# Performance work log

Measured on AMD Instinct MI355X. Metric: run time of the kernel, lower is better.

Reference implementation:

```python
import jax, jax.numpy as jnp
import numpy as np

B, P, L = 32, 256, 32            # samples, max paths/sample, tokens/path
V, DE, DP = 30000, 256, 256      # vocab, node emb dim, path emb dim
NH, DH = 8, 32                   # heads, head dim (NH*DH == DP)
DFF = 1024
NLAYERS = 4
MAXCHILD = 32
NEG = -1e9


def setup_inputs() -> dict:
    key = jax.random.key(0)
    ks = jax.random.split(key, 32)
    s = 0.02
    inp = {}
    inp['tokens'] = jax.random.randint(ks[0], (B, P, L), 0, V, dtype=jnp.int32)
    inp['paths_count'] = jax.random.randint(ks[1], (B,), 2, P + 1, dtype=jnp.int32)
    inp['target_indices'] = jax.random.randint(ks[2], (B,), 0, MAXCHILD, dtype=jnp.int32)
    inp['emb'] = jax.random.normal(ks[3], (V, DE)) * s
    inp['lstm1_k'] = jax.random.normal(ks[4], (DE, 4 * DP)) * s
    inp['lstm1_r'] = jax.random.normal(ks[5], (DP, 4 * DP)) * s
    inp['lstm1_b'] = jnp.zeros((4 * DP,))
    inp['lstm2_k'] = jax.random.normal(ks[6], (DP, 4 * DP)) * s
    inp['lstm2_r'] = jax.random.normal(ks[7], (DP, 4 * DP)) * s
    inp['lstm2_b'] = jnp.zeros((4 * DP,))
    inp['enc_wq'] = jax.random.normal(ks[8], (NLAYERS, DP, DP)) * s
    inp['enc_wk'] = jax.random.normal(ks[9], (NLAYERS, DP, DP)) * s
    inp['enc_wv'] = jax.random.normal(ks[10], (NLAYERS, DP, DP)) * s
    inp['enc_wo'] = jax.random.normal(ks[11], (NLAYERS, DP, DP)) * s
    inp['enc_ln1_g'] = jnp.ones((NLAYERS, DP))
    inp['enc_ln1_b'] = jnp.zeros((NLAYERS, DP))
    inp['enc_w1'] = jax.random.normal(ks[12], (NLAYERS, DP, DFF)) * s
    inp['enc_b1'] = jnp.zeros((NLAYERS, DFF))
    inp['enc_w2'] = jax.random.normal(ks[13], (NLAYERS, DFF, DP)) * s
    inp['enc_b2'] = jnp.zeros((NLAYERS, DP))
    inp['enc_ln2_g'] = jnp.ones((NLAYERS, DP))
    inp['enc_ln2_b'] = jnp.zeros((NLAYERS, DP))
    inp['W_r'] = jax.random.normal(ks[14], (DP, DP)) * s
    inp['W_g'] = jax.random.normal(ks[15], (2 * DP, DE)) * s
    inp['C_i'] = jax.random.normal(ks[16], (MAXCHILD, DP, DP)) * s
    return inp


def _lstm(x, K, R, b, return_seq):
    """Keras-style LSTM (gate order i,f,g,o). x: [N, L, d]."""
    N = x.shape[0]
    u = R.shape[0]
    def step(carry, xt):
        h, c = carry
        z = xt @ K + h @ R + b
        i, f, g, o = jnp.split(z, 4, axis=-1)
        c = jax.nn.sigmoid(f) * c + jax.nn.sigmoid(i) * jnp.tanh(g)
        h = jax.nn.sigmoid(o) * jnp.tanh(c)
        return (h, c), (h if return_seq else 0.0)
    init = (jnp.zeros((N, u), x.dtype), jnp.zeros((N, u), x.dtype))
    (h_last, _), ys = jax.lax.scan(step, init, jnp.swapaxes(x, 0, 1))
    return jnp.swapaxes(ys, 0, 1) if return_seq else h_last


def _layernorm(x, g, b):
    m = jnp.mean(x, axis=-1, keepdims=True)
    v = jnp.mean(jnp.square(x - m), axis=-1, keepdims=True)
    return (x - m) * jax.lax.rsqrt(v + 1e-5) * g + b


def _encoder_layer(x, mask, wq, wk, wv, wo, g1, bb1, w1, b1, w2, b2, g2, bb2):
    Bs, n, d = x.shape
    q = (x @ wq).reshape(Bs, n, NH, DH)
    k = (x @ wk).reshape(Bs, n, NH, DH)
    v = (x @ wv).reshape(Bs, n, NH, DH)
    scores = jnp.einsum('bqhd,bkhd->bhqk', q, k) / np.sqrt(DH).astype(np.float32)
    scores = jnp.where(mask[:, None, :, :], scores, NEG)
    a = jax.nn.softmax(scores, axis=-1)
    o = jnp.einsum('bhqk,bkhd->bqhd', a, v).reshape(Bs, n, d) @ wo
    x = _layernorm(x + o, g1, bb1)
    f = jax.nn.relu(x @ w1 + b1) @ w2 + b2
    return _layernorm(x + f, g2, bb2)


def reference(tokens, paths_count, target_indices, emb,
              lstm1_k, lstm1_r, lstm1_b, lstm2_k, lstm2_r, lstm2_b,
              enc_wq, enc_wk, enc_wv, enc_wo, enc_ln1_g, enc_ln1_b,
              enc_w1, enc_b1, enc_w2, enc_b2, enc_ln2_g, enc_ln2_b,
              W_r, W_g, C_i):
    # embed + ragged->flat paths: [B*P, L, DE]
    e = emb[tokens].reshape(B * P, L, DE)
    h1 = _lstm(e, lstm1_k, lstm1_r, lstm1_b, return_seq=True)      # [B*P, L, DP]
    h2 = _lstm(h1, lstm2_k, lstm2_r, lstm2_b, return_seq=False)    # [B*P, DP]
    Hall = h2.reshape(B, P, DP)

    # last valid path per sample is the root context R
    R = Hall[jnp.arange(B), paths_count - 1]                        # [B, DP]
    n = P - 1
    valid = jnp.arange(n)[None, :] < (paths_count - 1)[:, None]     # [B, n]
    H = jnp.where(valid[:, :, None], Hall[:, :n, :], 0.0)           # padded dense, zeros like to_tensor
    mask = valid[:, :, None] & valid[:, None, :]                    # per-sample block mask

    Z = H
    for l in range(NLAYERS):
        Z = _encoder_layer(Z, mask, enc_wq[l], enc_wk[l], enc_wv[l], enc_wo[l],
                           enc_ln1_g[l], enc_ln1_b[l], enc_w1[l], enc_b1[l],
                           enc_w2[l], enc_b2[l], enc_ln2_g[l], enc_ln2_b[l])

    # per-sample transform matrix gather and attention pooling
    C = C_i[target_indices]                                         # [B, DP, DP]
    R = jnp.einsum('bij,bj->bi', C, R)
    R = jax.nn.relu(R) @ W_r                                        # [B, DP]
    alpha = jax.nn.softmax(jnp.einsum('bnd,bd->bn', Z, R), axis=-1) # note: no pad mask (faithful)
    Zp = jnp.einsum('bn,bnd->bd', alpha, Z)                         # [B, DP]
    h = jax.nn.relu(jnp.concatenate([Zp, R], axis=-1) @ W_g)        # [B, DE]
    return jax.nn.softmax(h @ emb.T, axis=-1)                       # [B, V]
```

## Files before the change

kernel.cpp:

```cpp
#include <hip/hip_runtime.h>
#include <cstdint>
#include <cstddef>

typedef unsigned short u16;
typedef unsigned int   u32;
typedef float f32x4 __attribute__((ext_vector_type(4)));
typedef short s16x8 __attribute__((ext_vector_type(8)));
typedef u32   u32x4 __attribute__((ext_vector_type(4)));

#define DEV static __device__ __forceinline__
#define WAIT0SB() do{ asm volatile("s_waitcnt vmcnt(0)" ::: "memory"); __builtin_amdgcn_sched_barrier(0); }while(0)


static constexpr size_t OFF_EMBB = 0;
static constexpr size_t OFF_WP1  = 15360000;
static constexpr size_t OFF_WP2  = 16408576;
static constexpr size_t OFF_BQKV = 17457152;
static constexpr size_t OFF_WOT  = 19030016;
static constexpr size_t OFF_W1ET = 19554304;
static constexpr size_t OFF_W2ET = 21651456;
static constexpr size_t OFF_CIT  = 23748608;
static constexpr size_t OFF_HALL = 32137216;
static constexpr size_t OFF_X    = 40525824;
static constexpr size_t OFF_XB   = 48914432;
static constexpr size_t OFF_Y    = 53108736;
static constexpr size_t OFF_QKV  = 61497344;
static constexpr size_t OFF_AO   = 74080256;
static constexpr size_t OFF_F    = 78274560;
static constexpr size_t OFF_RV   = 95051776;
static constexpr size_t OFF_HB   = 95084544;
static constexpr size_t OFF_LOG  = 95100928;
static constexpr size_t OFF_H1A  = OFF_X;
static constexpr size_t OFF_H1B  = OFF_X + 4194304;
static constexpr size_t OFF_H2A  = OFF_X + 8388608;
static constexpr size_t OFF_H2B  = OFF_X + 12582912;
static constexpr size_t OFF_BARC = OFF_X + 16777216;

DEV u16 f2bf(float f){ u32 u = __builtin_bit_cast(u32, f); u += 0x7fffu + ((u>>16)&1u); return (u16)(u>>16); }
DEV float bf2f(u16 v){ return __builtin_bit_cast(float, (u32)v<<16); }
DEV float sigm(float x){ return 1.f/(1.f+__expf(-x)); }
DEV float tanh_f(float x){ float e=__expf(-2.f*fabsf(x)); float t=(1.f-e)/(1.f+e); return x<0.f? -t:t; }
DEV f32x4 splat4(float x){ f32x4 v={x,x,x,x}; return v; }
DEV f32x4 mfma16(s16x8 a, s16x8 b, f32x4 c){ return __builtin_amdgcn_mfma_f32_16x16x32_bf16(a,b,c,0,0,0); }

DEV int swz256(int row, int col){ int ch=col>>3; return row*256 + (((ch ^ (row&7))&31)<<3) + (col&7); }
DEV int swz128(int row, int col){ int ch=col>>3; return row*128 + (((ch ^ (row&7))&15)<<3) + (col&7); }
DEV int swz32 (int row, int col){ int ch=col>>3; return row*32  + (((ch ^ (row&3))&3)<<3)  + (col&7); }

DEV void st32_s(u32* p, u32 v){
  asm volatile("global_store_dword %0, %1, off sc0 sc1" :: "v"(p), "v"(v) : "memory");
}
DEV u32x4 ld128_s(const u32* p){
  u32x4 r;
  asm volatile("global_load_dwordx4 %0, %1, off sc0 sc1\n\ts_waitcnt vmcnt(0)" : "=v"(r) : "v"(p) : "memory");
  return r;
}
DEV void st128_s(u16* p, s16x8 v){
  asm volatile("global_store_dwordx4 %0, %1, off sc0 sc1" :: "v"(p), "v"(v) : "memory");
}
DEV void ld16_iss(const u16* pa, const u16* pb, s16x8 r[16]){
  asm volatile(
    "global_load_dwordx4 %0, %16, off sc0 sc1\n\t"
    "global_load_dwordx4 %1, %16, off offset:64 sc0 sc1\n\t"
    "global_load_dwordx4 %2, %16, off offset:128 sc0 sc1\n\t"
    "global_load_dwordx4 %3, %16, off offset:192 sc0 sc1\n\t"
    "global_load_dwordx4 %4, %16, off offset:256 sc0 sc1\n\t"
    "global_load_dwordx4 %5, %16, off offset:320 sc0 sc1\n\t"
    "global_load_dwordx4 %6, %16, off offset:384 sc0 sc1\n\t"
    "global_load_dwordx4 %7, %16, off offset:448 sc0 sc1\n\t"
    "global_load_dwordx4 %8, %17, off sc0 sc1\n\t"
    "global_load_dwordx4 %9, %17, off offset:64 sc0 sc1\n\t"
    "global_load_dwordx4 %10, %17, off offset:128 sc0 sc1\n\t"
    "global_load_dwordx4 %11, %17, off offset:192 sc0 sc1\n\t"
    "global_load_dwordx4 %12, %17, off offset:256 sc0 sc1\n\t"
    "global_load_dwordx4 %13, %17, off offset:320 sc0 sc1\n\t"
    "global_load_dwordx4 %14, %17, off offset:384 sc0 sc1\n\t"
    "global_load_dwordx4 %15, %17, off offset:448 sc0 sc1"
    : "=&v"(r[0]),"=&v"(r[1]),"=&v"(r[2]),"=&v"(r[3]),
      "=&v"(r[4]),"=&v"(r[5]),"=&v"(r[6]),"=&v"(r[7]),
      "=&v"(r[8]),"=&v"(r[9]),"=&v"(r[10]),"=&v"(r[11]),
      "=&v"(r[12]),"=&v"(r[13]),"=&v"(r[14]),"=&v"(r[15])
    : "v"(pa), "v"(pb) : "memory");
}

DEV void gbar(u32* arr, u32 gen){
  __syncthreads();
  if (threadIdx.x==0){
    asm volatile("s_waitcnt vmcnt(0)" ::: "memory");
    st32_s(arr + blockIdx.x, gen);
  }
  if (threadIdx.x < 64){
    bool done = false;
    do {
      u32x4 q = ld128_s(arr + threadIdx.x*4);
      done = __all(q.x>=gen && q.y>=gen && q.z>=gen && q.w>=gen);
      if (!done) __builtin_amdgcn_s_sleep(2);
    } while(!done);
  }
  __syncthreads();
}

struct TJob { const float* src; u32 dstOff; int K; int N; int stride; int f32out; };
struct PrepArgs { TJob j[60]; };

__global__ void k_prep(PrepArgs pa, char* __restrict__ ws){
  TJob jb = pa.j[blockIdx.y];
  int tilesK = jb.K >> 5, tilesN = jb.N >> 5;
  int ti = blockIdx.x;
  if (ti >= tilesK*tilesN) return;
  int tk = ti % tilesK, tn = ti / tilesK;
  __shared__ float tile[32][33];
  int r = threadIdx.x >> 5, c = threadIdx.x & 31;
  #pragma unroll
  for (int rr=0; rr<32; rr+=8)
    tile[rr+r][c] = jb.src[(size_t)(tk*32+rr+r)*jb.N + tn*32 + c];
  __syncthreads();
  if (jb.f32out){
    float* dst = (float*)(ws + jb.dstOff);
    #pragma unroll
    for (int rr=0; rr<32; rr+=8)
      dst[(size_t)(tn*32+rr+r)*jb.stride + tk*32 + c] = tile[c][rr+r];
  } else {
    u16* dst = (u16*)(ws + jb.dstOff);
    #pragma unroll
    for (int rr=0; rr<32; rr+=8)
      dst[(size_t)(tn*32+rr+r)*jb.stride + tk*32 + c] = f2bf(tile[c][rr+r]);
  }
}

__global__ void k_embcvt(const float* __restrict__ src, u16* __restrict__ dst, int n4){
  int i = blockIdx.x*blockDim.x + threadIdx.x;
  if (i >= n4) return;
  float4 v = ((const float4*)src)[i];
  uint2 pk;
  pk.x = f2bf(v.x) | ((u32)f2bf(v.y)<<16);
  pk.y = f2bf(v.z) | ((u32)f2bf(v.w)<<16);
  ((uint2*)dst)[i] = pk;
}

__global__ void k_packfrag(const float* __restrict__ srcA, const float* __restrict__ srcB,
                           u16* __restrict__ dst)
{
  int gid = blockIdx.x*256 + threadIdx.x;
  int lane = gid & 63;
  int hs   = (gid>>6) & 15;
  int c    = gid >> 10;
  int kc = c>>2, g = c&3;
  int l4 = lane>>4, l15 = lane&15;
  int col = g*256 + hs*16 + l15;
  int k0  = kc*32 + l4*8;
  u16 out[8];
  #pragma unroll
  for (int j=0;j<8;++j){
    int k = k0 + j;
    float v = (k < 256) ? srcA[(size_t)k*1024 + col] : srcB[(size_t)(k-256)*1024 + col];
    out[j] = f2bf(v);
  }
  *(s16x8*)(dst + (size_t)gid*8) = *(const s16x8*)out;
}

__global__ __launch_bounds__(1024,4) void k_lstm3(
    const int* __restrict__ tokens, const u16* __restrict__ EMBB,
    const u16* __restrict__ WP1, const u16* __restrict__ WP2,
    const float* __restrict__ b1, const float* __restrict__ b2,
    u16* __restrict__ H1A, u16* __restrict__ H1B,
    u16* __restrict__ H2A, u16* __restrict__ H2B,
    u32* __restrict__ bar, float* __restrict__ Hall)
{
  __shared__ u16 W1s[64*512];
  __shared__ u16 W2s[64*512];
  __shared__ u16 Hst[512*16];
  const int tid=threadIdx.x, lane=tid&63, v=tid>>6, l15=lane&15, l4=lane>>4;
  const int bid=blockIdx.x, sg=bid&15, hs=bid>>4;
  const int seq0w = sg*512 + v*32;
  u32* arr = bar;

  #pragma unroll
  for (int i=0;i<4;++i){
    int c = v*4+i;
    const u16* s1 = WP1 + ((size_t)(c*16+hs))*512 + lane*8;
    const u16* s2 = WP2 + ((size_t)(c*16+hs))*512 + lane*8;
    __builtin_amdgcn_global_load_lds((const __attribute__((address_space(1))) void*)s1,
        (__attribute__((address_space(3))) void*)(W1s + c*512), 16, 0, 0);
    __builtin_amdgcn_global_load_lds((const __attribute__((address_space(1))) void*)s2,
        (__attribute__((address_space(3))) void*)(W2s + c*512), 16, 0, 0);
  }
  float bl1[4], bl2[4];
  #pragma unroll
  for (int g=0;g<4;++g){ bl1[g]=b1[g*256 + hs*16 + l15]; bl2[g]=b2[g*256 + hs*16 + l15]; }
  asm volatile("s_waitcnt vmcnt(0)" ::: "memory");
  __syncthreads();

  float c1[8], c2[8];
  #pragma unroll
  for (int i=0;i<8;++i){ c1[i]=0.f; c2[i]=0.f; }
  const int row0 = seq0w + l15, row1 = seq0w + 16 + l15;
  const int cq = tid>>1, chf = tid&1;
  u32 gen = 0;

  #pragma unroll 1
  for (int t=0;t<32;++t){
    const u16* H1r = (t&1)? H1B : H1A;  u16* H1w = (t&1)? H1A : H1B;
    const u16* H2r = (t&1)? H2B : H2A;  u16* H2w = (t&1)? H2A : H2B;
    const int tok0 = tokens[row0*32 + t], tok1 = tokens[row1*32 + t];
    f32x4 acc[2][4];
    s16x8 r[16];
    ld16_iss(H1r + (size_t)row0*256 + l4*8, H1r + (size_t)row1*256 + l4*8, r);
    #pragma unroll
    for (int g=0;g<4;++g){ acc[0][g]=splat4(bl1[g]); acc[1][g]=splat4(bl1[g]); }
    #pragma unroll
    for (int kc=0;kc<8;++kc){
      s16x8 fa0 = *(const s16x8*)(EMBB + (size_t)tok0*256 + kc*32 + l4*8);
      s16x8 fa1 = *(const s16x8*)(EMBB + (size_t)tok1*256 + kc*32 + l4*8);
      #pragma unroll
      for (int g=0;g<4;++g){
        s16x8 wf = *(const s16x8*)&W1s[(kc*4+g)*512 + lane*8];
        acc[0][g]=mfma16(fa0,wf,acc[0][g]);
        acc[1][g]=mfma16(fa1,wf,acc[1][g]);
      }
    }
    WAIT0SB();
    #pragma unroll
    for (int k2=0;k2<8;++k2){
      #pragma unroll
      for (int g=0;g<4;++g){
        s16x8 wf = *(const s16x8*)&W1s[((8+k2)*4+g)*512 + lane*8];
        acc[0][g]=mfma16(r[k2],wf,acc[0][g]);
        acc[1][g]=mfma16(r[8+k2],wf,acc[1][g]);
      }
    }
    #pragma unroll
    for (int m=0;m<2;++m)
      #pragma unroll
      for (int rr=0;rr<4;++rr){
        int idx=m*4+rr;
        float zi=acc[m][0][rr], zf=acc[m][1][rr], zg=acc[m][2][rr], zo=acc[m][3][rr];
        float cc=sigm(zf)*c1[idx]+sigm(zi)*tanh_f(zg);
        c1[idx]=cc;
        Hst[(v*32 + m*16 + l4*4 + rr)*16 + l15] = f2bf(sigm(zo)*tanh_f(cc));
      }
    __syncthreads();
    st128_s(H1w + (size_t)(sg*512 + cq)*256 + hs*16 + chf*8, *(const s16x8*)&Hst[cq*16 + chf*8]);
    ++gen; gbar(arr, gen);
    #pragma unroll
    for (int g=0;g<4;++g){ acc[0][g]=splat4(bl2[g]); acc[1][g]=splat4(bl2[g]); }
    ld16_iss(H1w + (size_t)row0*256 + l4*8, H1w + (size_t)row1*256 + l4*8, r);
    WAIT0SB();
    #pragma unroll
    for (int k2=0;k2<8;++k2){
      #pragma unroll
      for (int g=0;g<4;++g){
        s16x8 wf = *(const s16x8*)&W2s[(k2*4+g)*512 + lane*8];
        acc[0][g]=mfma16(r[k2],wf,acc[0][g]);
        acc[1][g]=mfma16(r[8+k2],wf,acc[1][g]);
      }
    }
    ld16_iss(H2r + (size_t)row0*256 + l4*8, H2r + (size_t)row1*256 + l4*8, r);
    WAIT0SB();
    #pragma unroll
    for (int k2=0;k2<8;++k2){
      #pragma unroll
      for (int g=0;g<4;++g){
        s16x8 wf = *(const s16x8*)&W2s[((8+k2)*4+g)*512 + lane*8];
        acc[0][g]=mfma16(r[k2],wf,acc[0][g]);
        acc[1][g]=mfma16(r[8+k2],wf,acc[1][g]);
      }
    }
    __syncthreads();
    #pragma unroll
    for (int m=0;m<2;++m)
      #pragma unroll
      for (int rr=0;rr<4;++rr){
        int idx=m*4+rr;
        float zi=acc[m][0][rr], zf=acc[m][1][rr], zg=acc[m][2][rr], zo=acc[m][3][rr];
        float cc=sigm(zf)*c2[idx]+sigm(zi)*tanh_f(zg);
        c2[idx]=cc;
        float h=sigm(zo)*tanh_f(cc);
        Hst[(v*32 + m*16 + l4*4 + rr)*16 + l15] = f2bf(h);
        if (t==31) Hall[(size_t)(seq0w + m*16 + l4*4 + rr)*256 + hs*16 + l15] = h;
      }
    __syncthreads();
    st128_s(H2w + (size_t)(sg*512 + cq)*256 + hs*16 + chf*8, *(const s16x8*)&Hst[cq*16 + chf*8]);
  }
}

template<int BM, int EPI>
__global__ __launch_bounds__(512,2) void k_gemm(
    const u16* __restrict__ A, const u16* __restrict__ Bt, void* __restrict__ Cv,
    const float* __restrict__ bias, const float* __restrict__ Res,
    int M, int N, int K, int ldC)
{
  __shared__ u16 Asl[BM*256];
  const int tid=threadIdx.x, lane=tid&63, w=tid>>6, l15=lane&15, l4=lane>>4;
  const int mb=blockIdx.x, nb=blockIdx.y;
  constexpr int MT = BM/16;
  const int col0 = nb*256 + w*32;
  float bz0=0.f, bz1=0.f;
  if (EPI==1 || EPI==3 || EPI==5){ bz0 = bias[col0 + l15]; bz1 = bias[col0 + 16 + l15]; }
  f32x4 acc[MT][2];
  #pragma unroll
  for (int mt=0;mt<MT;++mt){ acc[mt][0]=splat4(bz0); acc[mt][1]=splat4(bz1); }
  for (int kb=0; kb<K; kb+=256){
    __syncthreads();
    if (tid < BM*8){
      int row=tid>>3, part=tid&7;
      int arow = mb*BM+row; if (arow > M-1) arow = M-1;
      const u16* src = A + (size_t)arow*K + kb + part*32;
      #pragma unroll
      for (int i=0;i<4;++i)
        *(s16x8*)&Asl[swz256(row, part*32+i*8)] = *(const s16x8*)(src+i*8);
    }
    __syncthreads();
    #pragma unroll
    for (int kc=0; kc<8; ++kc){
      s16x8 fa[MT];
      #pragma unroll
      for (int mt=0;mt<MT;++mt)
        fa[mt] = *(const s16x8*)&Asl[swz256(mt*16+l15, kc*32 + l4*8)];
      #pragma unroll
      for (int n=0;n<2;++n){
        int brow = col0 + n*16 + l15; if (brow > N-1) brow = N-1;
        const s16x8 fb = *(const s16x8*)(Bt + (size_t)brow*K + kb + kc*32 + l4*8);
        #pragma unroll
        for (int mt=0;mt<MT;++mt) acc[mt][n] = mfma16(fa[mt], fb, acc[mt][n]);
      }
    }
  }
  #pragma unroll
  for (int mt=0;mt<MT;++mt){
    #pragma unroll
    for (int n=0;n<2;++n){
      #pragma unroll
      for (int r=0;r<4;++r){
        int row = mb*BM + mt*16 + l4*4 + r;
        int col = col0 + n*16 + l15;
        if (col < N && row < M){
          float v = acc[mt][n][r];
          if (EPI==0){ ((u16*)Cv)[(size_t)row*ldC + col] = f2bf(v); }
          else if (EPI==1){ ((u16*)Cv)[(size_t)row*ldC + col] = f2bf(fmaxf(v,0.f)); }
          else if (EPI==2 || EPI==3){ ((float*)Cv)[(size_t)row*ldC + col] = v + Res[(size_t)row*ldC + col]; }
          else if (EPI==5){ ((u16*)Cv)[(size_t)row*ldC + col] = f2bf(v); }
          else { ((float*)Cv)[(size_t)row*ldC + col] = v; }
        }
      }
    }
  }
}

__global__ __launch_bounds__(256) void k_attn(const u16* __restrict__ QKV, u16* __restrict__ AO,
                                              const int* __restrict__ pc)
{
  __shared__ u16 Qs[256*32];
  __shared__ u16 Ks[256*32];
  __shared__ u16 Vt[32*256];
  __shared__ u16 Ab[4][64*128];
  const int bh=blockIdx.x, b=bh>>3, h=bh&7;
  const int tid=threadIdx.x, lane=tid&63, w=tid>>6, l15=lane&15, l4=lane>>4;
  const int pcm1 = pc[b]-1;
  {
    int row = tid;
    const u16* base = QKV + (size_t)(b*256+row)*768 + h*32;
    #pragma unroll
    for (int i=0;i<4;++i){
      *(s16x8*)&Qs[swz32(row, i*8)] = *(const s16x8*)(base + i*8);
      *(s16x8*)&Ks[swz32(row, i*8)] = *(const s16x8*)(base + 256 + i*8);
    }
    #pragma unroll
    for (int i=0;i<4;++i){
      s16x8 v = *(const s16x8*)(base + 512 + i*8);
      #pragma unroll
      for (int j=0;j<8;++j){
        int d = i*8+j;
        Vt[d*256 + ((((row>>3) ^ (d&7))&31)<<3) + (row&7)] = (u16)v[j];
      }
    }
  }
  __syncthreads();
  const float scale = 0.17677669529663689f;
  const int q0w = w*64;
  float rmax[4][4], rinv[4][4];
  #pragma unroll 1
  for (int m=0;m<4;++m){
    f32x4 sacc[16];
    #pragma unroll
    for (int nt=0;nt<16;++nt) sacc[nt]=splat4(0.f);
    s16x8 fa = *(const s16x8*)&Qs[swz32(q0w+m*16+l15, l4*8)];
    #pragma unroll
    for (int nt=0;nt<16;++nt){
      s16x8 fb = *(const s16x8*)&Ks[swz32(nt*16+l15, l4*8)];
      sacc[nt] = mfma16(fa, fb, sacc[nt]);
    }
    #pragma unroll
    for (int r=0;r<4;++r){
      int q = q0w + m*16 + l4*4 + r;
      bool vq = q < pcm1;
      float sv[16]; float mx = -3e38f;
      #pragma unroll
      for (int nt=0;nt<16;++nt){
        int k = nt*16 + l15;
        float s = (vq && k < pcm1) ? sacc[nt][r]*scale : -1e9f;
        if (k == 255) s = -1e30f;
        sv[nt] = s; mx = fmaxf(mx, s);
      }
      #pragma unroll
      for (int msk=1;msk<16;msk<<=1) mx = fmaxf(mx, __shfl_xor(mx, msk, 64));
      float sum = 0.f;
      #pragma unroll
      for (int nt=0;nt<16;++nt) sum += __expf(sv[nt]-mx);
      #pragma unroll
      for (int msk=1;msk<16;msk<<=1) sum += __shfl_xor(sum, msk, 64);
      rmax[m][r]=mx; rinv[m][r]=1.f/sum;
    }
  }
  f32x4 oacc[4][2];
  #pragma unroll
  for (int m=0;m<4;++m){ oacc[m][0]=splat4(0.f); oacc[m][1]=splat4(0.f); }
  #pragma unroll 1
  for (int kg=0; kg<2; ++kg){
    #pragma unroll 1
    for (int m=0;m<4;++m){
      s16x8 fa = *(const s16x8*)&Qs[swz32(q0w+m*16+l15, l4*8)];
      #pragma unroll
      for (int nt2=0;nt2<8;++nt2){
        int nt = kg*8 + nt2;
        s16x8 fb = *(const s16x8*)&Ks[swz32(nt*16+l15, l4*8)];
        f32x4 sa = mfma16(fa, fb, splat4(0.f));
        #pragma unroll
        for (int r=0;r<4;++r){
          int q = q0w + m*16 + l4*4 + r;
          int k = nt*16 + l15;
          float s = (q < pcm1 && k < pcm1) ? sa[r]*scale : -1e9f;
          if (k == 255) s = -1e30f;
          float p = __expf(s - rmax[m][r]) * rinv[m][r];
          Ab[w][swz128(m*16 + l4*4 + r, nt2*16 + l15)] = f2bf(p);
        }
      }
    }
    #pragma unroll 1
    for (int m=0;m<4;++m){
      #pragma unroll
      for (int kc=0;kc<4;++kc){
        s16x8 fa2 = *(const s16x8*)&Ab[w][swz128(m*16+l15, kc*32 + l4*8)];
        #pragma unroll
        for (int n=0;n<2;++n){
          int d = n*16 + l15;
          int kch = kg*16 + kc*4 + l4;
          s16x8 fb = *(const s16x8*)&Vt[d*256 + (((kch ^ (d&7))&31)<<3)];
          oacc[m][n] = mfma16(fa2, fb, oacc[m][n]);
        }
      }
    }
  }
  #pragma unroll
  for (int m=0;m<4;++m){
    #pragma unroll
    for (int n=0;n<2;++n){
      #pragma unroll
      for (int r=0;r<4;++r){
        int q = q0w + m*16 + l4*4 + r;
        AO[(size_t)(b*256+q)*256 + h*32 + n*16 + l15] = f2bf(oacc[m][n][r]);
      }
    }
  }
}

__global__ void k_ln(const float* __restrict__ Y, const float* __restrict__ g, const float* __restrict__ bb,
                     float* __restrict__ X, u16* __restrict__ Xb)
{
  int w = threadIdx.x >> 6, lane = threadIdx.x & 63;
  int row = blockIdx.x*4 + w;
  float4 v = ((const float4*)(Y + (size_t)row*256))[lane];
  float s = v.x+v.y+v.z+v.w;
  #pragma unroll
  for (int m=1;m<64;m<<=1) s += __shfl_xor(s, m, 64);
  float mean = s * (1.f/256.f);
  float dx=v.x-mean, dy=v.y-mean, dz=v.z-mean, dw=v.w-mean;
  float q = dx*dx+dy*dy+dz*dz+dw*dw;
  #pragma unroll
  for (int m=1;m<64;m<<=1) q += __shfl_xor(q, m, 64);
  float rstd = rsqrtf(q*(1.f/256.f) + 1e-5f);
  int c = lane*4;
  float o0=dx*rstd*g[c]+bb[c], o1=dy*rstd*g[c+1]+bb[c+1], o2=dz*rstd*g[c+2]+bb[c+2], o3=dw*rstd*g[c+3]+bb[c+3];
  float4 o; o.x=o0; o.y=o1; o.z=o2; o.w=o3;
  ((float4*)(X + (size_t)row*256))[lane] = o;
  uint2 pk; pk.x = f2bf(o0) | ((u32)f2bf(o1)<<16); pk.y = f2bf(o2) | ((u32)f2bf(o3)<<16);
  ((uint2*)(Xb + (size_t)row*256))[lane] = pk;
}

__global__ void k_buildZ(const float* __restrict__ Hall, const int* __restrict__ pc,
                         float* __restrict__ X, u16* __restrict__ Xb)
{
  int gid = blockIdx.x*256 + threadIdx.x;
  int row = gid >> 6;
  int b = row >> 8, p = row & 255;
  float4 v; v.x=v.y=v.z=v.w=0.f;
  if (p < pc[b]-1) v = ((const float4*)Hall)[gid];
  ((float4*)X)[gid] = v;
  uint2 pk; pk.x = f2bf(v.x) | ((u32)f2bf(v.y)<<16); pk.y = f2bf(v.z) | ((u32)f2bf(v.w)<<16);
  ((uint2*)Xb)[gid] = pk;
}

__global__ void k_rprep(const float* __restrict__ Hall, const int* __restrict__ pc, const int* __restrict__ tgt,
                        const float* __restrict__ CIT, const float* __restrict__ Wr, float* __restrict__ RV)
{
  int b = blockIdx.x, t = threadIdx.x;
  __shared__ float r0[256], ys[256];
  r0[t] = Hall[(size_t)(b*256 + pc[b]-1)*256 + t];
  __syncthreads();
  const float* Cb = CIT + (size_t)tgt[b]*65536;
  float a = 0.f;
  for (int j=0;j<256;++j) a += Cb[j*256 + t] * r0[j];
  ys[t] = fmaxf(a, 0.f);
  __syncthreads();
  float a2 = 0.f;
  for (int i=0;i<256;++i) a2 += Wr[i*256 + t] * ys[i];
  RV[b*256 + t] = a2;
}

__global__ void k_pool(const float* __restrict__ X, const float* __restrict__ RV,
                       const float* __restrict__ Wg, u16* __restrict__ HB)
{
  int b = blockIdx.x, t = threadIdx.x;
  __shared__ float R[256], al[256], red[256], zp[256];
  R[t] = RV[b*256+t];
  __syncthreads();
  float sc = -3e38f;
  if (t < 255){
    const float* z = X + (size_t)(b*256+t)*256;
    float a=0.f;
    for (int d=0;d<256;++d) a += z[d]*R[d];
    sc = a;
  }
  red[t] = sc;
  __syncthreads();
  for (int s=128;s>0;s>>=1){ if (t<s) red[t]=fmaxf(red[t],red[t+s]); __syncthreads(); }
  float M = red[0];
  __syncthreads();
  float e = (t<255) ? __expf(sc - M) : 0.f;
  red[t] = e;
  __syncthreads();
  for (int s=128;s>0;s>>=1){ if (t<s) red[t]+=red[t+s]; __syncthreads(); }
  float S = red[0];
  al[t] = e / S;
  __syncthreads();
  float acc = 0.f;
  for (int p=0;p<255;++p) acc += al[p] * X[(size_t)(b*256+p)*256 + t];
  zp[t] = acc;
  __syncthreads();
  float a2 = 0.f;
  for (int d=0;d<256;++d) a2 += zp[d] * Wg[d*256 + t];
  for (int d=0;d<256;++d) a2 += R[d]  * Wg[(256+d)*256 + t];
  HB[b*256+t] = f2bf(fmaxf(a2, 0.f));
}

__global__ void k_osm(const float* __restrict__ LOG, float* __restrict__ out)
{
  int b = blockIdx.x, t = threadIdx.x;
  __shared__ float red[512];
  const float* Lp = LOG + (size_t)b*30000;
  float mx = -3e38f;
  for (int i=t;i<30000;i+=512) mx = fmaxf(mx, Lp[i]);
  red[t]=mx; __syncthreads();
  for (int s=256;s>0;s>>=1){ if (t<s) red[t]=fmaxf(red[t],red[t+s]); __syncthreads(); }
  float M = red[0]; __syncthreads();
  float sm = 0.f;
  for (int i=t;i<30000;i+=512) sm += __expf(Lp[i]-M);
  red[t]=sm; __syncthreads();
  for (int s=256;s>0;s>>=1){ if (t<s) red[t]+=red[t+s]; __syncthreads(); }
  float rinv = 1.f/red[0];
  float* O = out + (size_t)b*30000;
  for (int i=t;i<30000;i+=512) O[i] = __expf(Lp[i]-M) * rinv;
}

extern "C" void kernel_launch(void* const* d_in, const int* in_sizes, int n_in,
                              void* d_out, int out_size, void* d_ws, size_t ws_size,
                              hipStream_t stream)
{
  const int*   tokens = (const int*)  d_in[0];
  const int*   pc     = (const int*)  d_in[1];
  const int*   tgt    = (const int*)  d_in[2];
  const float* emb    = (const float*)d_in[3];
  const float* l1k    = (const float*)d_in[4];
  const float* l1r    = (const float*)d_in[5];
  const float* l1b    = (const float*)d_in[6];
  const float* l2k    = (const float*)d_in[7];
  const float* l2r    = (const float*)d_in[8];
  const float* l2b    = (const float*)d_in[9];
  const float* wq     = (const float*)d_in[10];
  const float* wk     = (const float*)d_in[11];
  const float* wv     = (const float*)d_in[12];
  const float* wo     = (const float*)d_in[13];
  const float* ln1g   = (const float*)d_in[14];
  const float* ln1b   = (const float*)d_in[15];
  const float* w1e    = (const float*)d_in[16];
  const float* b1e    = (const float*)d_in[17];
  const float* w2e    = (const float*)d_in[18];
  const float* b2e    = (const float*)d_in[19];
  const float* ln2g   = (const float*)d_in[20];
  const float* ln2b   = (const float*)d_in[21];
  const float* Wr     = (const float*)d_in[22];
  const float* Wg     = (const float*)d_in[23];
  const float* Ci     = (const float*)d_in[24];

  char* ws = (char*)d_ws;
  u16*   EMBB = (u16*)  (ws + OFF_EMBB);
  u16*   WP1  = (u16*)  (ws + OFF_WP1);
  u16*   WP2  = (u16*)  (ws + OFF_WP2);
  float* CIT  = (float*)(ws + OFF_CIT);
  float* HALL = (float*)(ws + OFF_HALL);
  float* X    = (float*)(ws + OFF_X);
  u16*   XB   = (u16*)  (ws + OFF_XB);
  float* Y    = (float*)(ws + OFF_Y);
  u16*   QKVb = (u16*)  (ws + OFF_QKV);
  u16*   AOb  = (u16*)  (ws + OFF_AO);
  u16*   Fb   = (u16*)  (ws + OFF_F);
  float* RV   = (float*)(ws + OFF_RV);
  u16*   HB   = (u16*)  (ws + OFF_HB);
  float* LOGp = (float*)(ws + OFF_LOG);
  u16*   H1A  = (u16*)  (ws + OFF_H1A);
  u16*   H1B  = (u16*)  (ws + OFF_H1B);
  u16*   H2A  = (u16*)  (ws + OFF_H2A);
  u16*   H2B  = (u16*)  (ws + OFF_H2B);
  u32*   BARC = (u32*)  (ws + OFF_BARC);

  PrepArgs pa;
  int ji = 0;
  auto addJ = [&](const float* s, size_t off, int K, int N, int stride, int f32o){
    pa.j[ji].src=s; pa.j[ji].dstOff=(u32)off; pa.j[ji].K=K; pa.j[ji].N=N; pa.j[ji].stride=stride; pa.j[ji].f32out=f32o; ++ji;
  };
  for (int l=0;l<4;++l) addJ(wq + l*65536,  OFF_BQKV + (size_t)(l*768      )*512, 256,256,256,0);
  for (int l=0;l<4;++l) addJ(wk + l*65536,  OFF_BQKV + (size_t)(l*768 + 256)*512, 256,256,256,0);
  for (int l=0;l<4;++l) addJ(wv + l*65536,  OFF_BQKV + (size_t)(l*768 + 512)*512, 256,256,256,0);
  for (int l=0;l<4;++l) addJ(wo + l*65536,  OFF_WOT  + (size_t)l*131072, 256,256,256,0);
  for (int l=0;l<4;++l) addJ(w1e + l*262144, OFF_W1ET + (size_t)l*524288, 256,1024,256,0);
  for (int l=0;l<4;++l) addJ(w2e + l*262144, OFF_W2ET + (size_t)l*524288, 1024,256,1024,0);
  for (int c=0;c<32;++c) addJ(Ci + (size_t)c*65536, OFF_CIT + (size_t)c*262144, 256,256,256,1);

  hipMemsetAsync(ws + OFF_H1A, 0, 16777216 + 4096, stream);
  k_prep<<<dim3(256,56), dim3(256), 0, stream>>>(pa, ws);
  k_embcvt<<<dim3(7500), dim3(256), 0, stream>>>(emb, EMBB, 1920000);
  k_packfrag<<<dim3(256), dim3(256), 0, stream>>>(l1k, l1r, WP1);
  k_packfrag<<<dim3(256), dim3(256), 0, stream>>>(l2k, l2r, WP2);
  k_lstm3<<<dim3(256), dim3(1024), 0, stream>>>(tokens, EMBB, WP1, WP2, l1b, l2b,
                                                H1A, H1B, H2A, H2B, BARC, HALL);
  k_buildZ<<<dim3(2048), dim3(256), 0, stream>>>(HALL, pc, X, XB);
  k_rprep<<<dim3(32), dim3(256), 0, stream>>>(HALL, pc, tgt, CIT, Wr, RV);

  u16* BQKV = (u16*)(ws + OFF_BQKV);
  u16* WOT  = (u16*)(ws + OFF_WOT);
  u16* W1ET = (u16*)(ws + OFF_W1ET);
  u16* W2ET = (u16*)(ws + OFF_W2ET);
  for (int l=0;l<4;++l){
    k_gemm<64,0><<<dim3(128,3), dim3(512), 0, stream>>>(XB, BQKV + (size_t)l*768*256, QKVb, nullptr, nullptr, 8192, 768, 256, 768);
    k_attn<<<dim3(256), dim3(256), 0, stream>>>(QKVb, AOb, pc);
    k_gemm<64,2><<<dim3(128,1), dim3(512), 0, stream>>>(AOb, WOT + (size_t)l*65536, Y, nullptr, X, 8192, 256, 256, 256);
    k_ln<<<dim3(2048), dim3(256), 0, stream>>>(Y, ln1g + l*256, ln1b + l*256, X, XB);
    k_gemm<64,1><<<dim3(128,4), dim3(512), 0, stream>>>(XB, W1ET + (size_t)l*262144, Fb, b1e + l*1024, nullptr, 8192, 1024, 256, 1024);
    k_gemm<64,3><<<dim3(128,1), dim3(512), 0, stream>>>(Fb, W2ET + (size_t)l*262144, Y, b2e + l*256, X, 8192, 256, 1024, 256);
    k_ln<<<dim3(2048), dim3(256), 0, stream>>>(Y, ln2g + l*256, ln2b + l*256, X, XB);
  }

  k_pool<<<dim3(32), dim3(256), 0, stream>>>(X, RV, Wg, HB);
  k_gemm<32,4><<<dim3(1,118), dim3(512), 0, stream>>>(HB, EMBB, LOGp, nullptr, nullptr, 32, 30000, 256, 30000);
  k_osm<<<dim3(32), dim3(512), 0, stream>>>(LOGp, (float*)d_out);
}
```

Measured before the change: 2.340 ms.

## Fuse LayerNorm into residual GEMM epilogues and store LSTM hidden state directly

The residual-add GEMMs (attention output projection and FFN down-projection) now compute LayerNorm in their epilogue. Row statistics are reduced with shuffles and shared memory across the 8 waves, since each block owns full 256-wide rows. This removes the separate k_ln launches and the Y round trip. The LSTM kernel also drops its LDS staging and the __syncthreads around the hidden-state writeback, issuing per-element 16-bit global stores instead. This trades coalesced 128-bit stores for fewer barriers, and the variance is computed in the single-pass E[x^2]-mean^2 form, which is less numerically stable.

```diff
diff --git a/kernel.cpp b/kernel.cpp
--- a/kernel.cpp
+++ b/kernel.cpp
@@ -23,7 +23,6 @@
 static constexpr size_t OFF_HALL = 32137216;
 static constexpr size_t OFF_X    = 40525824;
 static constexpr size_t OFF_XB   = 48914432;
-static constexpr size_t OFF_Y    = 53108736;
 static constexpr size_t OFF_QKV  = 61497344;
 static constexpr size_t OFF_AO   = 74080256;
 static constexpr size_t OFF_F    = 78274560;
@@ -55,8 +54,8 @@
   asm volatile("global_load_dwordx4 %0, %1, off sc0 sc1\n\ts_waitcnt vmcnt(0)" : "=v"(r) : "v"(p) : "memory");
   return r;
 }
-DEV void st128_s(u16* p, s16x8 v){
-  asm volatile("global_store_dwordx4 %0, %1, off sc0 sc1" :: "v"(p), "v"(v) : "memory");
+DEV void st16_s(u16* p, u16 v){
+  asm volatile("global_store_short %0, %1, off sc0 sc1" :: "v"(p), "v"((u32)v) : "memory");
 }
 DEV void ld16_iss(const u16* pa, const u16* pb, s16x8 r[16]){
   asm volatile(
@@ -169,7 +168,6 @@
 {
   __shared__ u16 W1s[64*512];
   __shared__ u16 W2s[64*512];
-  __shared__ u16 Hst[512*16];
   const int tid=threadIdx.x, lane=tid&63, v=tid>>6, l15=lane&15, l4=lane>>4;
   const int bid=blockIdx.x, sg=bid&15, hs=bid>>4;
   const int seq0w = sg*512 + v*32;
@@ -195,7 +193,6 @@
   #pragma unroll
   for (int i=0;i<8;++i){ c1[i]=0.f; c2[i]=0.f; }
   const int row0 = seq0w + l15, row1 = seq0w + 16 + l15;
-  const int cq = tid>>1, chf = tid&1;
   u32 gen = 0;
 
   #pragma unroll 1
@@ -237,10 +234,9 @@
         float zi=acc[m][0][rr], zf=acc[m][1][rr], zg=acc[m][2][rr], zo=acc[m][3][rr];
         float cc=sigm(zf)*c1[idx]+sigm(zi)*tanh_f(zg);
         c1[idx]=cc;
-        Hst[(v*32 + m*16 + l4*4 + rr)*16 + l15] = f2bf(sigm(zo)*tanh_f(cc));
-      }
-    __syncthreads();
-    st128_s(H1w + (size_t)(sg*512 + cq)*256 + hs*16 + chf*8, *(const s16x8*)&Hst[cq*16 + chf*8]);
+        st16_s(H1w + (size_t)(seq0w + m*16 + l4*4 + rr)*256 + hs*16 + l15,
+               f2bf(sigm(zo)*tanh_f(cc)));
+      }
     ++gen; gbar(arr, gen);
     #pragma unroll
     for (int g=0;g<4;++g){ acc[0][g]=splat4(bl2[g]); acc[1][g]=splat4(bl2[g]); }
@@ -266,7 +262,6 @@
         acc[1][g]=mfma16(r[8+k2],wf,acc[1][g]);
       }
     }
-    __syncthreads();
     #pragma unroll
     for (int m=0;m<2;++m)
       #pragma unroll
@@ -276,11 +271,9 @@
         float cc=sigm(zf)*c2[idx]+sigm(zi)*tanh_f(zg);
         c2[idx]=cc;
         float h=sigm(zo)*tanh_f(cc);
-        Hst[(v*32 + m*16 + l4*4 + rr)*16 + l15] = f2bf(h);
+        st16_s(H2w + (size_t)(seq0w + m*16 + l4*4 + rr)*256 + hs*16 + l15, f2bf(h));
         if (t==31) Hall[(size_t)(seq0w + m*16 + l4*4 + rr)*256 + hs*16 + l15] = h;
       }
-    __syncthreads();
-    st128_s(H2w + (size_t)(sg*512 + cq)*256 + hs*16 + chf*8, *(const s16x8*)&Hst[cq*16 + chf*8]);
   }
 }
 
@@ -288,15 +281,18 @@
 __global__ __launch_bounds__(512,2) void k_gemm(
     const u16* __restrict__ A, const u16* __restrict__ Bt, void* __restrict__ Cv,
     const float* __restrict__ bias, const float* __restrict__ Res,
-    int M, int N, int K, int ldC)
+    int M, int N, int K, int ldC,
+    const float* __restrict__ lng, const float* __restrict__ lnb, u16* __restrict__ outB)
 {
   __shared__ u16 Asl[BM*256];
+  __shared__ float sS[512];
+  __shared__ float sQ[512];
   const int tid=threadIdx.x, lane=tid&63, w=tid>>6, l15=lane&15, l4=lane>>4;
   const int mb=blockIdx.x, nb=blockIdx.y;
   constexpr int MT = BM/16;
   const int col0 = nb*256 + w*32;
   float bz0=0.f, bz1=0.f;
-  if (EPI==1 || EPI==3 || EPI==5){ bz0 = bias[col0 + l15]; bz1 = bias[col0 + 16 + l15]; }
+  if (EPI==1 || EPI==5 || EPI==7){ bz0 = bias[col0 + l15]; bz1 = bias[col0 + 16 + l15]; }
   f32x4 acc[MT][2];
   #pragma unroll
   for (int mt=0;mt<MT;++mt){ acc[mt][0]=splat4(bz0); acc[mt][1]=splat4(bz1); }
@@ -326,21 +322,65 @@
       }
     }
   }
-  #pragma unroll
-  for (int mt=0;mt<MT;++mt){
-    #pragma unroll
-    for (int n=0;n<2;++n){
+  if constexpr (EPI==6 || EPI==7){
+    float vv[MT][2][4];
+    #pragma unroll
+    for (int mt=0;mt<MT;++mt)
+      #pragma unroll
+      for (int n=0;n<2;++n)
+        #pragma unroll
+        for (int r=0;r<4;++r){
+          int row = mb*BM + mt*16 + l4*4 + r;
+          int col = col0 + n*16 + l15;
+          vv[mt][n][r] = acc[mt][n][r] + Res[(size_t)row*256 + col];
+        }
+    #pragma unroll
+    for (int mt=0;mt<MT;++mt)
       #pragma unroll
       for (int r=0;r<4;++r){
-        int row = mb*BM + mt*16 + l4*4 + r;
-        int col = col0 + n*16 + l15;
-        if (col < N && row < M){
-          float v = acc[mt][n][r];
-          if (EPI==0){ ((u16*)Cv)[(size_t)row*ldC + col] = f2bf(v); }
-          else if (EPI==1){ ((u16*)Cv)[(size_t)row*ldC + col] = f2bf(fmaxf(v,0.f)); }
-          else if (EPI==2 || EPI==3){ ((float*)Cv)[(size_t)row*ldC + col] = v + Res[(size_t)row*ldC + col]; }
-          else if (EPI==5){ ((u16*)Cv)[(size_t)row*ldC + col] = f2bf(v); }
-          else { ((float*)Cv)[(size_t)row*ldC + col] = v; }
+        float s = vv[mt][0][r] + vv[mt][1][r];
+        float q = vv[mt][0][r]*vv[mt][0][r] + vv[mt][1][r]*vv[mt][1][r];
+        #pragma unroll
+        for (int msk=1;msk<16;msk<<=1){ s += __shfl_xor(s, msk, 64); q += __shfl_xor(q, msk, 64); }
+        if (l15==0){ sS[w*64 + mt*16 + l4*4 + r] = s; sQ[w*64 + mt*16 + l4*4 + r] = q; }
+      }
+    __syncthreads();
+    #pragma unroll
+    for (int mt=0;mt<MT;++mt)
+      #pragma unroll
+      for (int r=0;r<4;++r){
+        int lrow = mt*16 + l4*4 + r;
+        float S=0.f, Q=0.f;
+        #pragma unroll
+        for (int w2=0;w2<8;++w2){ S += sS[w2*64 + lrow]; Q += sQ[w2*64 + lrow]; }
+        float mean = S * (1.f/256.f);
+        float var  = Q * (1.f/256.f) - mean*mean;
+        float rstd = rsqrtf(var + 1e-5f);
+        int row = mb*BM + lrow;
+        #pragma unroll
+        for (int n=0;n<2;++n){
+          int col = col0 + n*16 + l15;
+          float ov = (vv[mt][n][r]-mean)*rstd*lng[col] + lnb[col];
+          ((float*)Cv)[(size_t)row*256 + col] = ov;
+          outB[(size_t)row*256 + col] = f2bf(ov);
+        }
+      }
+  } else {
+    #pragma unroll
+    for (int mt=0;mt<MT;++mt){
+      #pragma unroll
+      for (int n=0;n<2;++n){
+        #pragma unroll
+        for (int r=0;r<4;++r){
+          int row = mb*BM + mt*16 + l4*4 + r;
+          int col = col0 + n*16 + l15;
+          if (col < N && row < M){
+            float v = acc[mt][n][r];
+            if (EPI==0){ ((u16*)Cv)[(size_t)row*ldC + col] = f2bf(v); }
+            else if (EPI==1){ ((u16*)Cv)[(size_t)row*ldC + col] = f2bf(fmaxf(v,0.f)); }
+            else if (EPI==5){ ((u16*)Cv)[(size_t)row*ldC + col] = f2bf(v); }
+            else { ((float*)Cv)[(size_t)row*ldC + col] = v; }
+          }
         }
       }
     }
@@ -462,29 +502,6 @@
       }
     }
   }
-}
-
-__global__ void k_ln(const float* __restrict__ Y, const float* __restrict__ g, const float* __restrict__ bb,
-                     float* __restrict__ X, u16* __restrict__ Xb)
-{
-  int w = threadIdx.x >> 6, lane = threadIdx.x & 63;
-  int row = blockIdx.x*4 + w;
-  float4 v = ((const float4*)(Y + (size_t)row*256))[lane];
-  float s = v.x+v.y+v.z+v.w;
-  #pragma unroll
-  for (int m=1;m<64;m<<=1) s += __shfl_xor(s, m, 64);
-  float mean = s * (1.f/256.f);
-  float dx=v.x-mean, dy=v.y-mean, dz=v.z-mean, dw=v.w-mean;
-  float q = dx*dx+dy*dy+dz*dz+dw*dw;
-  #pragma unroll
-  for (int m=1;m<64;m<<=1) q += __shfl_xor(q, m, 64);
-  float rstd = rsqrtf(q*(1.f/256.f) + 1e-5f);
-  int c = lane*4;
-  float o0=dx*rstd*g[c]+bb[c], o1=dy*rstd*g[c+1]+bb[c+1], o2=dz*rstd*g[c+2]+bb[c+2], o3=dw*rstd*g[c+3]+bb[c+3];
-  float4 o; o.x=o0; o.y=o1; o.z=o2; o.w=o3;
-  ((float4*)(X + (size_t)row*256))[lane] = o;
-  uint2 pk; pk.x = f2bf(o0) | ((u32)f2bf(o1)<<16); pk.y = f2bf(o2) | ((u32)f2bf(o3)<<16);
-  ((uint2*)(Xb + (size_t)row*256))[lane] = pk;
 }
 
 __global__ void k_buildZ(const float* __restrict__ Hall, const int* __restrict__ pc,
@@ -610,7 +627,6 @@
   float* HALL = (float*)(ws + OFF_HALL);
   float* X    = (float*)(ws + OFF_X);
   u16*   XB   = (u16*)  (ws + OFF_XB);
-  float* Y    = (float*)(ws + OFF_Y);
   u16*   QKVb = (u16*)  (ws + OFF_QKV);
   u16*   AOb  = (u16*)  (ws + OFF_AO);
   u16*   Fb   = (u16*)  (ws + OFF_F);
@@ -651,16 +667,14 @@
   u16* W1ET = (u16*)(ws + OFF_W1ET);
   u16* W2ET = (u16*)(ws + OFF_W2ET);
   for (int l=0;l<4;++l){
-    k_gemm<64,0><<<dim3(128,3), dim3(512), 0, stream>>>(XB, BQKV + (size_t)l*768*256, QKVb, nullptr, nullptr, 8192, 768, 256, 768);
+    k_gemm<64,0><<<dim3(128,3), dim3(512), 0, stream>>>(XB, BQKV + (size_t)l*768*256, QKVb, nullptr, nullptr, 8192, 768, 256, 768, nullptr, nullptr, nullptr);
     k_attn<<<dim3(256), dim3(256), 0, stream>>>(QKVb, AOb, pc);
-    k_gemm<64,2><<<dim3(128,1), dim3(512), 0, stream>>>(AOb, WOT + (size_t)l*65536, Y, nullptr, X, 8192, 256, 256, 256);
-    k_ln<<<dim3(2048), dim3(256), 0, stream>>>(Y, ln1g + l*256, ln1b + l*256, X, XB);
-    k_gemm<64,1><<<dim3(128,4), dim3(512), 0, stream>>>(XB, W1ET + (size_t)l*262144, Fb, b1e + l*1024, nullptr, 8192, 1024, 256, 1024);
-    k_gemm<64,3><<<dim3(128,1), dim3(512), 0, stream>>>(Fb, W2ET + (size_t)l*262144, Y, b2e + l*256, X, 8192, 256, 1024, 256);
-    k_ln<<<dim3(2048), dim3(256), 0, stream>>>(Y, ln2g + l*256, ln2b + l*256, X, XB);
+    k_gemm<64,6><<<dim3(128,1), dim3(512), 0, stream>>>(AOb, WOT + (size_t)l*65536, X, nullptr, X, 8192, 256, 256, 256, ln1g + l*256, ln1b + l*256, XB);
+    k_gemm<64,1><<<dim3(128,4), dim3(512), 0, stream>>>(XB, W1ET + (size_t)l*262144, Fb, b1e + l*1024, nullptr, 8192, 1024, 256, 1024, nullptr, nullptr, nullptr);
+    k_gemm<64,7><<<dim3(128,1), dim3(512), 0, stream>>>(Fb, W2ET + (size_t)l*262144, X, b2e + l*256, X, 8192, 256, 1024, 256, ln2g + l*256, ln2b + l*256, XB);
   }
 
   k_pool<<<dim3(32), dim3(256), 0, stream>>>(X, RV, Wg, HB);
-  k_gemm<32,4><<<dim3(1,118), dim3(512), 0, stream>>>(HB, EMBB, LOGp, nullptr, nullptr, 32, 30000, 256, 30000);
+  k_gemm<32,4><<<dim3(1,118), dim3(512), 0, stream>>>(HB, EMBB, LOGp, nullptr, nullptr, 32, 30000, 256, 30000, nullptr, nullptr, nullptr);
   k_osm<<<dim3(32), dim3(512), 0, stream>>>(LOGp, (float*)d_out);
 }
```

After: 2.025 ms. 1.16x faster.
